# Kernel optimization log

Hardware: AMD Instinct MI355X
Metric: run time of the kernel (lower is better)

Reference implementation:

```python
import jax, jax.numpy as jnp
import numpy as np

N_SEGMENT = 8
N_DIV = 8
C = 256            # net.in_channels
O = 256            # net.out_channels (1x1 conv)
NT, H, W = 128, 28, 28


def _make_shift_weights():
    """Replicates MsCEGroupConv1d.weight_init(); returns per-channel temporal
    kernels as [channels, k] float32 arrays (cross-correlation taps)."""
    planes = C // 4
    fold = planes // N_DIV
    w3 = np.zeros((C // 2, 3), np.float32)
    w3[:2 * fold, 0] = 1.0
    w3[2 * fold:4 * fold, 2] = 1.0
    w3[4 * fold:, 1] = 1.0
    w5 = np.zeros((planes, 5), np.float32)
    w5[:fold, :2] = 1.0
    w5[fold:2 * fold, 3:] = 1.0
    w5[2 * fold:, 2] = 1.0
    w7 = np.zeros((planes, 7), np.float32)
    w7[:fold, :3] = 1.0
    w7[fold:2 * fold, 4:] = 1.0
    w7[2 * fold:, 3] = 1.0
    return jnp.asarray(w3), jnp.asarray(w5), jnp.asarray(w7)


def setup_inputs() -> dict:
    key = jax.random.key(0)
    k1, k2, k3 = jax.random.split(key, 3)
    x = jax.random.normal(k1, (NT, C, H, W), dtype=jnp.float32)
    w3, w5, w7 = _make_shift_weights()
    # wrapped net: 1x1 Conv2d(C -> O) with bias (PyTorch default init scale)
    bound = 1.0 / np.sqrt(C)
    net_w = jax.random.uniform(k2, (O, C), jnp.float32, -bound, bound)
    net_b = jax.random.uniform(k3, (O,), jnp.float32, -bound, bound)
    return {"x": x, "w3": w3, "w5": w5, "w7": w7, "net_w": net_w, "net_b": net_b}


def _dwconv_t(x, w):
    """Depthwise temporal conv. x: [nb, c, T, h, w], w: [c, k], 'same' padding.
    Matches torch Conv3d(kernel=(k,1,1), padding=(k//2,0,0), groups=c)."""
    k = w.shape[1]
    p = k // 2
    T = x.shape[2]
    xp = jnp.pad(x, ((0, 0), (0, 0), (p, p), (0, 0), (0, 0)))
    out = w[None, :, 0, None, None, None] * jax.lax.dynamic_slice_in_dim(xp, 0, T, axis=2)
    for i in range(1, k):
        out = out + w[None, :, i, None, None, None] * jax.lax.dynamic_slice_in_dim(xp, i, T, axis=2)
    return out


def reference(x, w3, w5, w7, net_w, net_b):
    nt, c, h, w = x.shape
    nb = nt // N_SEGMENT
    # [nt,c,h,w] -> [nb, c, T, h, w]
    xt = x.reshape(nb, N_SEGMENT, c, h, w).transpose(0, 2, 1, 3, 4)
    x3 = xt[:, : c // 2]
    x5 = xt[:, c // 2 : c // 2 + c // 4]
    x7 = xt[:, c // 2 + c // 4 :]
    y3 = _dwconv_t(x3, w3)
    y5 = _dwconv_t(x5, w5)
    y7 = _dwconv_t(x7, w7)
    y = jnp.concatenate([y3, y5, y7], axis=1)        # [nb, c, T, h, w]
    y = y.transpose(0, 2, 1, 3, 4).reshape(nt, c, h, w)
    # net: 1x1 Conv2d
    out = jnp.einsum('nchw,oc->nohw', y, net_w) + net_b[None, :, None, None]
    return out
```

## Files before the change

### kernel.cpp

```cpp
#include <hip/hip_runtime.h>
#include <hip/hip_bf16.h>

typedef __attribute__((ext_vector_type(8))) short short8;
typedef __attribute__((ext_vector_type(4))) float f32x4;
typedef __attribute__((ext_vector_type(4))) unsigned int u32x4;

#define C_TOT 256
#define O_TOT 256
#define HW_   784
#define NT_   128
#define KMAX  1792
#define KPAD_STD 320
#define XBYTES (NT_ * C_TOT * HW_ * 4)
#define MARKER 0x60000000u

#define WS_IDX_OFF  16
#define WS_CVAL_OFF (WS_IDX_OFF + 4 * KMAX)
#define WS_OFFT_OFF (WS_CVAL_OFF + 4 * KMAX)
#define WS_A3_OFF   (WS_OFFT_OFF + 4 * 8 * KMAX)
#define WS_ZERO_OFF (WS_A3_OFF + 512 * KMAX)

#if __has_builtin(__builtin_amdgcn_global_load_lds)
#define USE_DMA 1
#else
#define USE_DMA 0
#endif

__device__ __forceinline__ unsigned int pk2(float lo, float hi) {
    float2 f; f.x = lo; f.y = hi;
    __hip_bfloat162 h = __float22bfloat162_rn(f);
    unsigned int r;
    __builtin_memcpy(&r, &h, 4);
    return r;
}
__device__ __forceinline__ unsigned short f2b(float f) {
    union { float f; unsigned int u; } cv; cv.f = f;
    unsigned int u = cv.u;
    u += 0x7fffu + ((u >> 16) & 1u);
    return (unsigned short)(u >> 16);
}

__global__ __launch_bounds__(256)
void build_idx(const float* __restrict__ w3, const float* __restrict__ w5,
               const float* __restrict__ w7, unsigned int* __restrict__ meta,
               unsigned int* __restrict__ idx, float* __restrict__ cval,
               unsigned int* __restrict__ offt, float* __restrict__ zpage)
{
    const int c = threadIdx.x;
    zpage[c] = 0.f;

    float cf[7];
    #pragma unroll
    for (int i = 0; i < 7; ++i) cf[i] = 0.f;
    if (c < 128) {
        #pragma unroll
        for (int i = 0; i < 3; ++i) cf[i + 2] = w3[c * 3 + i];
    } else if (c < 192) {
        #pragma unroll
        for (int i = 0; i < 5; ++i) cf[i + 1] = w5[(c - 128) * 5 + i];
    } else {
        #pragma unroll
        for (int i = 0; i < 7; ++i) cf[i] = w7[(c - 192) * 7 + i];
    }
    int cnt = 0;
    #pragma unroll
    for (int i = 0; i < 7; ++i) cnt += (cf[i] != 0.f);

    __shared__ int sc[256];
    sc[c] = cnt;
    __syncthreads();
    for (int off = 1; off < 256; off <<= 1) {
        int u = 0;
        if (c >= off) u = sc[c - off];
        __syncthreads();
        sc[c] += u;
        __syncthreads();
    }
    const int start = sc[c] - cnt;
    int J = sc[255];
    if (J > KMAX) J = KMAX;
    int Kpad = (J + 31) & ~31;
    if (Kpad > KMAX) Kpad = KMAX;
    if (c == 0) { meta[0] = (unsigned int)Kpad; meta[1] = (unsigned int)J; }

    int j = start;
    #pragma unroll
    for (int i = 0; i < 7; ++i) {
        if (cf[i] != 0.f) {
            if (j < KMAX) {
                idx[j] = (unsigned int)c | ((unsigned int)i << 8);
                cval[j] = cf[i];
                const int dt  = i - 3;
                const int lin = (dt * C_TOT + c) * (HW_ * 4);
                #pragma unroll
                for (int tt = 0; tt < 8; ++tt) {
                    const int tf = tt + dt;
                    offt[tt * KMAX + j] =
                        (tf >= 0 && tf < 8) ? (unsigned int)lin : MARKER;
                }
            }
            ++j;
        }
    }
    for (int p = J + c; p < Kpad; p += 256) {
        idx[p] = 3u << 8;
        cval[p] = 0.f;
        #pragma unroll
        for (int tt = 0; tt < 8; ++tt) offt[tt * KMAX + p] = MARKER;
    }
}

__global__ __launch_bounds__(256)
void build_A3(const float* __restrict__ netw, const unsigned int* __restrict__ meta,
              const unsigned int* __restrict__ idx, const float* __restrict__ cval,
              unsigned short* __restrict__ A3)
{
    const int o = blockIdx.x;
    const int Kpad   = (int)meta[0];
    const int nslots = Kpad >> 3;
    for (int s = threadIdx.x; s < nslots; s += 256) {
        unsigned short v[8];
        #pragma unroll
        for (int e = 0; e < 8; ++e) {
            const int jj = s * 8 + e;
            const int c  = (int)(idx[jj] & 255u);
            v[e] = f2b(netw[o * C_TOT + c] * cval[jj]);
        }
        *reinterpret_cast<u32x4*>(&A3[((size_t)s * 256 + o) * 8]) =
            *reinterpret_cast<const u32x4*>(v);
    }
}

__global__ __launch_bounds__(256, 2)
void msce_dma(const float* __restrict__ x,
              const unsigned short* __restrict__ A3,
              const unsigned int* __restrict__ offt,
              const unsigned int* __restrict__ meta,
              const float* __restrict__ net_b,
              const float* __restrict__ zpage,
              float* __restrict__ out)
{
    __shared__ unsigned int Bl[3][2080];

    const int Kpad = (int)meta[0];
    const int tid  = threadIdx.x;
    const int w    = tid >> 6;
    const int lane = tid & 63;

    const int bid  = blockIdx.x;
    const int work = (bid & 7) * 208 + (bid >> 3);
    const int n    = work / 13;
    const int tile = work - n * 13;
    const int p0   = (tile < 12) ? tile * 64 : 720;
    const int t    = n & 7;

    const int koct = lane >> 4;
    const int prow = lane & 15;
    const unsigned int pc16  = (unsigned int)(prow * 16);
    const unsigned int n_off = (unsigned int)n * (unsigned int)(C_TOT * HW_ * 4);
    const unsigned int p04   = (unsigned int)(p0 * 4);
    const unsigned int* offrow = offt + (size_t)t * KMAX;

    f32x4 acc[4][4];
    #pragma unroll
    for (int ms = 0; ms < 4; ++ms) {
        const f32x4 b = *reinterpret_cast<const f32x4*>(
                            &net_b[w * 64 + ms * 16 + koct * 4]);
        #pragma unroll
        for (int ns = 0; ns < 4; ++ns) acc[ms][ns] = b;
    }

    auto ldaf = [&](int kk, short8* af) {
        const unsigned short* abase =
            A3 + ((size_t)(kk * 4 + koct) * 256 + w * 64 + prow) * 8;
        #pragma unroll
        for (int ms = 0; ms < 4; ++ms)
            af[ms] = *reinterpret_cast<const short8*>(abase + (size_t)ms * 128);
    };

    auto comp = [&](int bsel, const short8* af) {
        const int rowbase = koct * 520;
        #pragma unroll
        for (int ns = 0; ns < 4; ++ns) {
            const int cb = ns * 16 + prow;
            float gg[8];
            #pragma unroll
            for (int e = 0; e < 8; ++e)
                gg[e] = __builtin_bit_cast(float,
                    Bl[bsel][rowbase + (e >> 2) * 260 + (e & 3) * 64 + cb]);
            u32x4 bw;
            bw[0] = pk2(gg[0], gg[1]);
            bw[1] = pk2(gg[2], gg[3]);
            bw[2] = pk2(gg[4], gg[5]);
            bw[3] = pk2(gg[6], gg[7]);
            const short8 bfr = __builtin_bit_cast(short8, bw);
            #pragma unroll
            for (int ms = 0; ms < 4; ++ms)
                acc[ms][ns] = __builtin_amdgcn_mfma_f32_16x16x32_bf16(
                                  af[ms], bfr, acc[ms][ns], 0, 0, 0);
        }
    };

#if USE_DMA
    if (Kpad == KPAD_STD) {
        unsigned int offa[20];
        #pragma unroll
        for (int i = 0; i < 20; ++i)
            offa[i] = offrow[(i >> 1) * 32 + w * 8 + (i & 1) * 4 + koct];

        const char* xb = (const char*)x;
        const char* zb = (const char*)zpage;

        auto stage1 = [&](unsigned int off, int buf, int q) {
            const char* src = (off != MARKER)
                            ? xb + (n_off + off + p04 + pc16)
                            : zb + pc16;
            unsigned int* dst = &Bl[buf][(w * 2 + q) * 260];
            __builtin_amdgcn_global_load_lds(
                (const __attribute__((address_space(1))) unsigned int*)src,
                (__attribute__((address_space(3))) unsigned int*)dst, 16, 0, 0);
        };

        short8 af0[4], af1[4];

        stage1(offa[0], 0, 0); stage1(offa[1], 0, 1);
        stage1(offa[2], 1, 0); stage1(offa[3], 1, 1);
        ldaf(0, af0);

#define BAR1() do { \
    asm volatile("s_waitcnt lgkmcnt(0)" ::: "memory"); \
    __builtin_amdgcn_s_barrier(); \
    __builtin_amdgcn_sched_barrier(0); } while (0)
#define BAR2(VN) do { \
    asm volatile("s_waitcnt vmcnt(" #VN ")" ::: "memory"); \
    __builtin_amdgcn_s_barrier(); \
    __builtin_amdgcn_sched_barrier(0); } while (0)
#define STEP(KK, VN, AFC, AFN) do { \
    BAR1(); \
    if ((KK) + 2 < 10) { \
        stage1(offa[2 * ((KK) + 2)],     ((KK) + 2) % 3, 0); \
        stage1(offa[2 * ((KK) + 2) + 1], ((KK) + 2) % 3, 1); \
    } \
    if ((KK) + 1 < 10) ldaf((KK) + 1, AFN); \
    BAR2(VN); \
    comp((KK) % 3, AFC); } while (0)

        STEP(0, 12, af0, af1);
        STEP(1, 12, af1, af0);
        STEP(2, 12, af0, af1);
        STEP(3, 12, af1, af0);
        STEP(4, 12, af0, af1);
        STEP(5, 12, af1, af0);
        STEP(6, 12, af0, af1);
        STEP(7, 12, af1, af0);
        STEP(8, 10, af0, af1);
        STEP(9, 4, af1, af0);
#undef STEP
#undef BAR2
#undef BAR1
    } else
#endif
    {
        const int KK = Kpad >> 5;
        for (int kk = 0; kk < KK; ++kk) {
            unsigned int o8[8];
            #pragma unroll
            for (int e = 0; e < 8; ++e)
                o8[e] = offrow[kk * 32 + koct * 8 + e];
            short8 af[4];
            ldaf(kk, af);
            #pragma unroll
            for (int ns = 0; ns < 4; ++ns) {
                const unsigned int pofs = n_off + (unsigned int)((p0 + ns * 16 + prow) * 4);
                float g[8];
                #pragma unroll
                for (int e = 0; e < 8; ++e) {
                    const unsigned int of = o8[e] + pofs;
                    g[e] = (o8[e] != MARKER && of < (unsigned int)XBYTES)
                         ? x[of >> 2] : 0.f;
                }
                u32x4 bw;
                bw[0] = pk2(g[0], g[1]);
                bw[1] = pk2(g[2], g[3]);
                bw[2] = pk2(g[4], g[5]);
                bw[3] = pk2(g[6], g[7]);
                const short8 bfr = __builtin_bit_cast(short8, bw);
                #pragma unroll
                for (int ms = 0; ms < 4; ++ms)
                    acc[ms][ns] = __builtin_amdgcn_mfma_f32_16x16x32_bf16(
                                      af[ms], bfr, acc[ms][ns], 0, 0, 0);
            }
        }
    }

    #pragma unroll
    for (int ns = 0; ns < 4; ++ns) {
        const int p = p0 + ns * 16 + prow;
        #pragma unroll
        for (int ms = 0; ms < 4; ++ms) {
            const int o = w * 64 + ms * 16 + koct * 4;
            const size_t base = ((size_t)n * O_TOT + o) * HW_ + p;
            #pragma unroll
            for (int r = 0; r < 4; ++r)
                out[base + (size_t)r * HW_] = acc[ms][ns][r];
        }
    }
}

extern "C" void kernel_launch(void* const* d_in, const int* in_sizes, int n_in,
                              void* d_out, int out_size, void* d_ws, size_t ws_size,
                              hipStream_t stream) {
    const float* x    = (const float*)d_in[0];
    const float* w3p  = (const float*)d_in[1];
    const float* w5p  = (const float*)d_in[2];
    const float* w7p  = (const float*)d_in[3];
    const float* netw = (const float*)d_in[4];
    const float* netb = (const float*)d_in[5];
    float* outp = (float*)d_out;

    char* ws = (char*)d_ws;
    unsigned int*   meta  = (unsigned int*)ws;
    unsigned int*   idx   = (unsigned int*)(ws + WS_IDX_OFF);
    float*          cval  = (float*)(ws + WS_CVAL_OFF);
    unsigned int*   offt  = (unsigned int*)(ws + WS_OFFT_OFF);
    unsigned short* A3    = (unsigned short*)(ws + WS_A3_OFF);
    float*          zpage = (float*)(ws + WS_ZERO_OFF);

    hipLaunchKernelGGL(build_idx, dim3(1), dim3(256), 0, stream,
                       w3p, w5p, w7p, meta, idx, cval, offt, zpage);
    hipLaunchKernelGGL(build_A3, dim3(256), dim3(256), 0, stream,
                       netw, meta, idx, cval, A3);

    hipLaunchKernelGGL(msce_dma, dim3(1664), dim3(256), 0, stream,
                       x, A3, offt, meta, netb, zpage, outp);
}
```

Baseline: 52.20 us.

## Use 4-deep LDS ring to drop per-step barrier and stage offsets in LDS

Result: slower. 53.49 us (+2.5%).

```diff
diff --git a/kernel.cpp b/kernel.cpp
--- a/kernel.cpp
+++ b/kernel.cpp
@@ -131,7 +131,7 @@
     }
 }
 
-__global__ __launch_bounds__(256, 2)
+__global__ __launch_bounds__(256, 3)
 void msce_dma(const float* __restrict__ x,
               const unsigned short* __restrict__ A3,
               const unsigned int* __restrict__ offt,
@@ -140,7 +140,8 @@
               const float* __restrict__ zpage,
               float* __restrict__ out)
 {
-    __shared__ unsigned int Bl[3][2080];
+    __shared__ unsigned int Bl[4][2080];
+    __shared__ unsigned int s_off[KPAD_STD];
 
     const int Kpad = (int)meta[0];
     const int tid  = threadIdx.x;
@@ -156,6 +157,7 @@
 
     const int koct = lane >> 4;
     const int prow = lane & 15;
+    const int w8   = w * 8;
     const unsigned int pc16  = (unsigned int)(prow * 16);
     const unsigned int n_off = (unsigned int)n * (unsigned int)(C_TOT * HW_ * 4);
     const unsigned int p04   = (unsigned int)(p0 * 4);
@@ -203,11 +205,6 @@
 
 #if USE_DMA
     if (Kpad == KPAD_STD) {
-        unsigned int offa[20];
-        #pragma unroll
-        for (int i = 0; i < 20; ++i)
-            offa[i] = offrow[(i >> 1) * 32 + w * 8 + (i & 1) * 4 + koct];
-
         const char* xb = (const char*)x;
         const char* zb = (const char*)zpage;
 
@@ -221,43 +218,46 @@
                 (__attribute__((address_space(3))) unsigned int*)dst, 16, 0, 0);
         };
 
+        for (int i = tid; i < KPAD_STD; i += 256) s_off[i] = offrow[i];
+        __syncthreads();
+
+        unsigned int so0[2], so1[2];
+        {
+            const unsigned int q00 = s_off[w8 + koct],      q01 = s_off[w8 + 4 + koct];
+            const unsigned int q10 = s_off[32 + w8 + koct], q11 = s_off[32 + w8 + 4 + koct];
+            so0[0] = s_off[64 + w8 + koct];  so0[1] = s_off[64 + w8 + 4 + koct];
+            stage1(q00, 0, 0); stage1(q01, 0, 1);
+            stage1(q10, 1, 0); stage1(q11, 1, 1);
+        }
         short8 af0[4], af1[4];
-
-        stage1(offa[0], 0, 0); stage1(offa[1], 0, 1);
-        stage1(offa[2], 1, 0); stage1(offa[3], 1, 1);
         ldaf(0, af0);
 
-#define BAR1() do { \
-    asm volatile("s_waitcnt lgkmcnt(0)" ::: "memory"); \
-    __builtin_amdgcn_s_barrier(); \
-    __builtin_amdgcn_sched_barrier(0); } while (0)
-#define BAR2(VN) do { \
+#define STEP(KK, VN, AFC, AFN, SOC, SON) do { \
+    if ((KK) + 1 < 10) ldaf((KK) + 1, AFN); \
+    if ((KK) + 2 < 10) { \
+        stage1(SOC[0], ((KK) + 2) & 3, 0); \
+        stage1(SOC[1], ((KK) + 2) & 3, 1); \
+    } \
+    if ((KK) + 3 < 10) { \
+        SON[0] = s_off[((KK) + 3) * 32 + w8 + koct]; \
+        SON[1] = s_off[((KK) + 3) * 32 + w8 + 4 + koct]; \
+    } \
     asm volatile("s_waitcnt vmcnt(" #VN ")" ::: "memory"); \
     __builtin_amdgcn_s_barrier(); \
-    __builtin_amdgcn_sched_barrier(0); } while (0)
-#define STEP(KK, VN, AFC, AFN) do { \
-    BAR1(); \
-    if ((KK) + 2 < 10) { \
-        stage1(offa[2 * ((KK) + 2)],     ((KK) + 2) % 3, 0); \
-        stage1(offa[2 * ((KK) + 2) + 1], ((KK) + 2) % 3, 1); \
-    } \
-    if ((KK) + 1 < 10) ldaf((KK) + 1, AFN); \
-    BAR2(VN); \
-    comp((KK) % 3, AFC); } while (0)
-
-        STEP(0, 12, af0, af1);
-        STEP(1, 12, af1, af0);
-        STEP(2, 12, af0, af1);
-        STEP(3, 12, af1, af0);
-        STEP(4, 12, af0, af1);
-        STEP(5, 12, af1, af0);
-        STEP(6, 12, af0, af1);
-        STEP(7, 12, af1, af0);
-        STEP(8, 10, af0, af1);
-        STEP(9, 4, af1, af0);
+    __builtin_amdgcn_sched_barrier(0); \
+    comp((KK) & 3, AFC); } while (0)
+
+        STEP(0, 12, af0, af1, so0, so1);
+        STEP(1, 12, af1, af0, so1, so0);
+        STEP(2, 12, af0, af1, so0, so1);
+        STEP(3, 12, af1, af0, so1, so0);
+        STEP(4, 12, af0, af1, so0, so1);
+        STEP(5, 12, af1, af0, so1, so0);
+        STEP(6, 12, af0, af1, so0, so1);
+        STEP(7, 12, af1, af0, so1, so0);
+        STEP(8, 10, af0, af1, so0, so1);
+        STEP(9, 4, af1, af0, so1, so0);
 #undef STEP
-#undef BAR2
-#undef BAR1
     } else
 #endif
     {
```
